# Performance work log

Measured on AMD Instinct MI355X. Metric: run time of the kernel, lower is better.

The kernel has to match this reference:

```python
import jax, jax.numpy as jnp
import numpy as np

EPS = 1e-6
C = 0.05            # curvature
TEMPERATURE = 0.1
ALPHA_D = 0.5       # current_epoch = 0 -> alpha stays at init value


def setup_inputs() -> dict:
    key = jax.random.key(0)
    k1, k2 = jax.random.split(key)
    B, D = 1024, 128
    # scale so norms stay well inside the Poincare ball (radius 1/sqrt(c) ~ 4.47)
    z_hyp = jax.random.normal(k1, (B, D), dtype=jnp.float32) * 0.05
    z_hyp_prime = jax.random.normal(k2, (B, D), dtype=jnp.float32) * 0.05
    return {"z_hyp": z_hyp, "z_hyp_prime": z_hyp_prime}


def _pairwise_hyp_distance(zx, zy, c):
    """d(x_i, y_j) = 2/sqrt(c) * atanh(sqrt(c) * ||mobius_add(-x_i, y_j)||) for all pairs."""
    x = -zx[:, None, :]          # [B, 1, D]  (neg_x in the original)
    y = zy[None, :, :]           # [1, B, D]
    x2 = jnp.sum(x * x, axis=-1, keepdims=True)   # [B, 1, 1]
    y2 = jnp.sum(y * y, axis=-1, keepdims=True)   # [1, B, 1]
    xy = jnp.sum(x * y, axis=-1, keepdims=True)   # [B, B, 1]
    num = (1.0 + 2.0 * c * xy + c * y2) * x + (1.0 - c * x2) * y   # [B, B, D]
    den = jnp.maximum(1.0 + 2.0 * c * xy + (c ** 2) * x2 * y2, EPS)
    m = num / den
    mnorm = jnp.sqrt(jnp.sum(m * m, axis=-1))      # [B, B]
    sqrt_c = np.sqrt(c).astype(np.float32)
    return (2.0 / sqrt_c) * jnp.arctanh(jnp.minimum(sqrt_c * mnorm, 1.0 - EPS))


def reference(z_hyp, z_hyp_prime):
    B = z_hyp.shape[0]
    distances = _pairwise_hyp_distance(z_hyp, z_hyp_prime, C)      # [B, B]
    distance_sim = -distances / TEMPERATURE

    # angle-based similarity (cosine, F.normalize with eps=1e-12)
    zn = z_hyp / jnp.maximum(jnp.linalg.norm(z_hyp, axis=1, keepdims=True), 1e-12)
    zpn = z_hyp_prime / jnp.maximum(jnp.linalg.norm(z_hyp_prime, axis=1, keepdims=True), 1e-12)
    angle_sim = (zn @ zpn.T) / TEMPERATURE

    combined_sim = ALPHA_D * distance_sim + (1.0 - ALPHA_D) * angle_sim

    # unsupervised InfoNCE-style loss: positives on the diagonal, diagonal
    # excluded from the denominator (faithful to the original code)
    pos_sim = jnp.diagonal(combined_sim)                           # [B]
    exp_sim = jnp.exp(combined_sim) * (1.0 - jnp.eye(B, dtype=combined_sim.dtype))
    denom = jnp.sum(exp_sim, axis=1)                               # [B]
    loss = jnp.mean(-pos_sim + jnp.log(denom))
    return loss
```

## Files before the change

kernel.cpp:

```cpp
#include <hip/hip_runtime.h>
#include <math.h>

#define B_ROWS 1024
#define D_DIM 128
#define DCHUNKS 32

__device__ __forceinline__ float dot4(float4 a, float4 b) {
  return fmaf(a.x, b.x, fmaf(a.y, b.y, fmaf(a.z, b.z, a.w * b.w)));
}

#define K_C 0.05f
#define K_SQRT_C 0.22360679774997896f
#define K_INV_SQRT_C 4.47213595499958f
#define K_EPS 1e-6f
#define K_HALF_INV_T 5.0f

__global__ __launch_bounds__(1024) void hypcd_pair(const float* __restrict__ za,
                                                   const float* __restrict__ zb,
                                                   float* __restrict__ row_loss) {
  __shared__ float s_a[4 * D_DIM];
  __shared__ float s_x2[4];
  __shared__ float s_pos[4];
  __shared__ float s_esum[4];

  const int tid = threadIdx.x;
  const int i0 = blockIdx.x * 4;

  if (tid < (4 * D_DIM / 4)) {
    reinterpret_cast<float4*>(s_a)[tid] =
        reinterpret_cast<const float4*>(za + (size_t)i0 * D_DIM)[tid];
  }
  if (tid < 4) s_esum[tid] = 0.0f;
  __syncthreads();

  const int wave = tid >> 6;
  const int lane = tid & 63;

  if (wave < 4) {
    float v0 = s_a[wave * D_DIM + lane];
    float v1 = s_a[wave * D_DIM + lane + 64];
    float s = fmaf(v0, v0, v1 * v1);
#pragma unroll
    for (int m = 32; m >= 1; m >>= 1) s += __shfl_xor(s, m);
    if (lane == 0) s_x2[wave] = s;
  }
  __syncthreads();

  float x2v[4], rnxv[4];
#pragma unroll
  for (int i = 0; i < 4; ++i) {
    x2v[i] = s_x2[i];
    rnxv[i] = 1.0f / fmaxf(sqrtf(x2v[i]), 1e-12f);
  }

  const int dg = lane & 7;
  const int jg = lane >> 3;
  const int b0 = dg & 1, b1 = (dg >> 1) & 1, b2 = (dg >> 2) & 1;
  const int pbase = (b0 << 3) | (b1 << 2) | (b2 << 1);
  const int isel = pbase >> 2;
  const int jj0 = pbase & 3;

  const float x2i = b0 ? (b1 ? x2v[3] : x2v[2]) : (b1 ? x2v[1] : x2v[0]);
  const float rnxi = b0 ? (b1 ? rnxv[3] : rnxv[2]) : (b1 ? rnxv[1] : rnxv[0]);

  float my_esum = 0.0f;
  const float4* bp = reinterpret_cast<const float4*>(zb);

#pragma unroll
  for (int pass = 0; pass < 2; ++pass) {
    const int jb = pass * 512 + wave * 32 + jg * 4;

    float v[16];
    float y2p[4];
#pragma unroll
    for (int k = 0; k < 16; ++k) v[k] = 0.0f;
#pragma unroll
    for (int k = 0; k < 4; ++k) y2p[k] = 0.0f;

#pragma unroll
    for (int dstep = 0; dstep < 4; ++dstep) {
      const int dc = dstep * 8 + dg;
      float4 bv0 = bp[(jb + 0) * DCHUNKS + dc];
      float4 bv1 = bp[(jb + 1) * DCHUNKS + dc];
      float4 bv2 = bp[(jb + 2) * DCHUNKS + dc];
      float4 bv3 = bp[(jb + 3) * DCHUNKS + dc];
#pragma unroll
      for (int i = 0; i < 4; ++i) {
        float4 av = reinterpret_cast<const float4*>(s_a + i * D_DIM)[dc];
        v[i * 4 + 0] += dot4(av, bv0);
        v[i * 4 + 1] += dot4(av, bv1);
        v[i * 4 + 2] += dot4(av, bv2);
        v[i * 4 + 3] += dot4(av, bv3);
      }
      y2p[0] += dot4(bv0, bv0);
      y2p[1] += dot4(bv1, bv1);
      y2p[2] += dot4(bv2, bv2);
      y2p[3] += dot4(bv3, bv3);
    }

#pragma unroll
    for (int m = 1; m < 8; m <<= 1) {
#pragma unroll
      for (int k = 0; k < 4; ++k) y2p[k] += __shfl_xor(y2p[k], m);
    }

    float w8[8];
#pragma unroll
    for (int k = 0; k < 8; ++k) {
      float mine = b0 ? v[8 + k] : v[k];
      float theirs = b0 ? v[k] : v[8 + k];
      w8[k] = mine + __shfl_xor(theirs, 1);
    }
    float w4[4];
#pragma unroll
    for (int k = 0; k < 4; ++k) {
      float mine = b1 ? w8[4 + k] : w8[k];
      float theirs = b1 ? w8[k] : w8[4 + k];
      w4[k] = mine + __shfl_xor(theirs, 2);
    }
    float w2[2];
#pragma unroll
    for (int k = 0; k < 2; ++k) {
      float mine = b2 ? w4[2 + k] : w4[k];
      float theirs = b2 ? w4[k] : w4[2 + k];
      w2[k] = mine + __shfl_xor(theirs, 4);
    }

    const float y2s0 = b2 ? y2p[2] : y2p[0];
    const float y2s1 = b2 ? y2p[3] : y2p[1];

#pragma unroll
    for (int pp = 0; pp < 2; ++pp) {
      const float g = (pp == 0) ? w2[0] : w2[1];
      const float y2 = (pp == 0) ? y2s0 : y2s1;
      const int gj = jb + jj0 + pp;
      const int gi = i0 + isel;

      const float xy = -g;
      const float Am = 1.0f + 2.0f * K_C * xy + K_C * y2;
      const float Bm = 1.0f - K_C * x2i;
      const float den = fmaxf(1.0f + 2.0f * K_C * xy + K_C * K_C * x2i * y2, K_EPS);
      const float num2 = Am * Am * x2i + 2.0f * Am * Bm * xy + Bm * Bm * y2;
      const float mnorm = sqrtf(fmaxf(num2, 0.0f)) / den;
      const float t = fminf(K_SQRT_C * mnorm, 1.0f - K_EPS);
      const float dist = K_INV_SQRT_C * logf((1.0f + t) / (1.0f - t));
      const float rny = 1.0f / fmaxf(sqrtf(y2), 1e-12f);
      const float comb = K_HALF_INV_T * (g * rnxi * rny - dist);

      if (gi == gj) {
        s_pos[isel] = comb;
      } else {
        my_esum += expf(comb);
      }
    }
  }

#pragma unroll
  for (int m = 8; m <= 32; m <<= 1) my_esum += __shfl_xor(my_esum, m);
  if (jg == 0) atomicAdd(&s_esum[isel], my_esum);
  __syncthreads();

  if (tid < 4) {
    row_loss[i0 + tid] = logf(s_esum[tid]) - s_pos[tid];
  }
}

__global__ __launch_bounds__(256) void hypcd_reduce(const float* __restrict__ row_loss,
                                                    float* __restrict__ out) {
  __shared__ float s[4];
  const int tid = threadIdx.x;
  float v = row_loss[tid] + row_loss[tid + 256] + row_loss[tid + 512] +
            row_loss[tid + 768];
#pragma unroll
  for (int m = 32; m >= 1; m >>= 1) v += __shfl_xor(v, m);
  if ((tid & 63) == 0) s[tid >> 6] = v;
  __syncthreads();
  if (tid == 0) out[0] = (s[0] + s[1] + s[2] + s[3]) * (1.0f / 1024.0f);
}

extern "C" void kernel_launch(void* const* d_in, const int* in_sizes, int n_in,
                              void* d_out, int out_size, void* d_ws, size_t ws_size,
                              hipStream_t stream) {
  const float* za = (const float*)d_in[0];
  const float* zb = (const float*)d_in[1];
  float* row_loss = (float*)d_ws;

  hypcd_pair<<<B_ROWS / 4, 1024, 0, stream>>>(za, zb, row_loss);
  hypcd_reduce<<<1, 256, 0, stream>>>(row_loss, (float*)d_out);
}
```

Measured before the change: 65.92 us.

## Fuse final reduction via atomicAdd, use fast math intrinsics, trim y2 shuffles

Removes the separate reduce kernel: each block writes its partial mean to the output with an atomicAdd, and the output is zeroed with a memset on the stream. Replaces exact sqrt, divide, log and exp with rsqrt and fast __logf, __expf and __fdividef intrinsics, and folds the arithmetic into fmaf. Cuts the y2 butterfly reduction to two values per lane. This trades a kernel launch for a memset plus 256 atomics, leaves a nondeterministic summation order, and uses slightly less accurate transcendentals.

Result: slower. 68.17 us (+3.4%).

```diff
diff --git a/kernel.cpp b/kernel.cpp
--- a/kernel.cpp
+++ b/kernel.cpp
@@ -17,11 +17,12 @@
 
 __global__ __launch_bounds__(1024) void hypcd_pair(const float* __restrict__ za,
                                                    const float* __restrict__ zb,
-                                                   float* __restrict__ row_loss) {
+                                                   float* __restrict__ out) {
   __shared__ float s_a[4 * D_DIM];
   __shared__ float s_x2[4];
   __shared__ float s_pos[4];
   __shared__ float s_esum[4];
+  __shared__ float s_rl[4];
 
   const int tid = threadIdx.x;
   const int i0 = blockIdx.x * 4;
@@ -50,7 +51,7 @@
 #pragma unroll
   for (int i = 0; i < 4; ++i) {
     x2v[i] = s_x2[i];
-    rnxv[i] = 1.0f / fmaxf(sqrtf(x2v[i]), 1e-12f);
+    rnxv[i] = __frsqrt_rn(fmaxf(x2v[i], 1e-24f));
   }
 
   const int dg = lane & 7;
@@ -98,11 +99,21 @@
       y2p[3] += dot4(bv3, bv3);
     }
 
+    {
+      float q0keep = b2 ? y2p[2] : y2p[0];
+      float q0send = b2 ? y2p[0] : y2p[2];
+      float q1keep = b2 ? y2p[3] : y2p[1];
+      float q1send = b2 ? y2p[1] : y2p[3];
+      y2p[0] = q0keep + __shfl_xor(q0send, 4);
+      y2p[1] = q1keep + __shfl_xor(q1send, 4);
 #pragma unroll
-    for (int m = 1; m < 8; m <<= 1) {
-#pragma unroll
-      for (int k = 0; k < 4; ++k) y2p[k] += __shfl_xor(y2p[k], m);
+      for (int m = 1; m <= 2; m <<= 1) {
+        y2p[0] += __shfl_xor(y2p[0], m);
+        y2p[1] += __shfl_xor(y2p[1], m);
+      }
     }
+    const float y2s0 = y2p[0];
+    const float y2s1 = y2p[1];
 
     float w8[8];
 #pragma unroll
@@ -126,9 +137,6 @@
       w2[k] = mine + __shfl_xor(theirs, 4);
     }
 
-    const float y2s0 = b2 ? y2p[2] : y2p[0];
-    const float y2s1 = b2 ? y2p[3] : y2p[1];
-
 #pragma unroll
     for (int pp = 0; pp < 2; ++pp) {
       const float g = (pp == 0) ? w2[0] : w2[1];
@@ -137,20 +145,22 @@
       const int gi = i0 + isel;
 
       const float xy = -g;
-      const float Am = 1.0f + 2.0f * K_C * xy + K_C * y2;
-      const float Bm = 1.0f - K_C * x2i;
-      const float den = fmaxf(1.0f + 2.0f * K_C * xy + K_C * K_C * x2i * y2, K_EPS);
-      const float num2 = Am * Am * x2i + 2.0f * Am * Bm * xy + Bm * Bm * y2;
-      const float mnorm = sqrtf(fmaxf(num2, 0.0f)) / den;
+      const float Am = fmaf(2.0f * K_C, xy, fmaf(K_C, y2, 1.0f));
+      const float Bm = fmaf(-K_C, x2i, 1.0f);
+      const float den =
+          fmaxf(fmaf(2.0f * K_C, xy, fmaf(K_C * K_C * x2i, y2, 1.0f)), K_EPS);
+      const float num2 =
+          fmaf(Am * Am, x2i, fmaf(2.0f * Am * Bm, xy, Bm * Bm * y2));
+      const float mnorm = __fdividef(sqrtf(fmaxf(num2, 0.0f)), den);
       const float t = fminf(K_SQRT_C * mnorm, 1.0f - K_EPS);
-      const float dist = K_INV_SQRT_C * logf((1.0f + t) / (1.0f - t));
-      const float rny = 1.0f / fmaxf(sqrtf(y2), 1e-12f);
-      const float comb = K_HALF_INV_T * (g * rnxi * rny - dist);
+      const float dist = K_INV_SQRT_C * __logf(__fdividef(1.0f + t, 1.0f - t));
+      const float rny = __frsqrt_rn(fmaxf(y2, 1e-24f));
+      const float comb = K_HALF_INV_T * fmaf(g * rnxi, rny, -dist);
 
       if (gi == gj) {
         s_pos[isel] = comb;
       } else {
-        my_esum += expf(comb);
+        my_esum += __expf(comb);
       }
     }
   }
@@ -161,21 +171,12 @@
   __syncthreads();
 
   if (tid < 4) {
-    row_loss[i0 + tid] = logf(s_esum[tid]) - s_pos[tid];
+    s_rl[tid] = __logf(s_esum[tid]) - s_pos[tid];
   }
-}
-
-__global__ __launch_bounds__(256) void hypcd_reduce(const float* __restrict__ row_loss,
-                                                    float* __restrict__ out) {
-  __shared__ float s[4];
-  const int tid = threadIdx.x;
-  float v = row_loss[tid] + row_loss[tid + 256] + row_loss[tid + 512] +
-            row_loss[tid + 768];
-#pragma unroll
-  for (int m = 32; m >= 1; m >>= 1) v += __shfl_xor(v, m);
-  if ((tid & 63) == 0) s[tid >> 6] = v;
   __syncthreads();
-  if (tid == 0) out[0] = (s[0] + s[1] + s[2] + s[3]) * (1.0f / 1024.0f);
+  if (tid == 0) {
+    atomicAdd(out, (s_rl[0] + s_rl[1] + s_rl[2] + s_rl[3]) * (1.0f / 1024.0f));
+  }
 }
 
 extern "C" void kernel_launch(void* const* d_in, const int* in_sizes, int n_in,
@@ -183,8 +184,6 @@
                               hipStream_t stream) {
   const float* za = (const float*)d_in[0];
   const float* zb = (const float*)d_in[1];
-  float* row_loss = (float*)d_ws;
-
-  hypcd_pair<<<B_ROWS / 4, 1024, 0, stream>>>(za, zb, row_loss);
-  hypcd_reduce<<<1, 256, 0, stream>>>(row_loss, (float*)d_out);
+  (void)hipMemsetAsync(d_out, 0, sizeof(float), stream);
+  hypcd_pair<<<B_ROWS / 4, 1024, 0, stream>>>(za, zb, (float*)d_out);
 }
```
